# Optimization experiments

Measured on AMD Instinct MI355X. Metric: run time of the kernel, lower is better.

The kernel has to match this reference:

```python
import jax, jax.numpy as jnp
import numpy as np

NLAYERS, NHID, NOUT, BSZ, STEPS = 4, 1024, 512, 64, 128


def setup_inputs() -> dict:
    key = jax.random.key(0)
    k0, k1, k2, k3, k4 = jax.random.split(key, 5)
    stdv = 1.0 / np.sqrt(NHID).astype(np.float32)
    hx = jax.random.normal(k0, (NLAYERS, BSZ, NHID), jnp.float32)
    cx = jax.random.normal(k1, (NLAYERS, BSZ, NHID), jnp.float32)
    W = jax.random.uniform(k2, (NLAYERS - 1, 4 * NHID, NHID), jnp.float32, -stdv, stdv)
    U = jax.random.uniform(k3, (NLAYERS, 4 * NHID, NHID), jnp.float32, -stdv, stdv)
    L = jax.random.uniform(k4, (NOUT, NHID), jnp.float32, -stdv, stdv)
    return {"hx": hx, "cx": cx, "W": W, "U": U, "L": L, "steps": STEPS}


def _lstm_cell(igates, hgates, cx):
    # PyTorch fused LSTM gate order: input, forget, cell, output
    g = igates + hgates
    i, f, c, o = jnp.split(g, 4, axis=-1)
    i = jax.nn.sigmoid(i)
    f = jax.nn.sigmoid(f)
    c = jnp.tanh(c)
    o = jax.nn.sigmoid(o)
    cy = f * cx + i * c
    hy = o * jnp.tanh(cy)
    return hy, cy


def reference(hx, cx, W, U, L, steps):
    nlayers, bsz, nhid = hx.shape
    out0 = hx[-1] @ L.T  # initial projection of top-layer hidden -> [bsz, nout]

    def step(carry, _):
        h, c = carry
        # hidden-to-gate GEMM for all layers at once: [L,B,4H]
        hgates = jnp.einsum('lbh,lgh->lbg', h, U)
        hy_list, cy_list = [], []
        prev = jnp.zeros((bsz, 4 * nhid), h.dtype)  # layer-0 input gates are zeros
        for i in range(nlayers):
            igates = prev if i == 0 else hy_list[-1] @ W[i - 1].T
            hy, cy = _lstm_cell(igates, hgates[i], c[i])
            hy_list.append(hy)
            cy_list.append(cy)
        hn = jnp.stack(hy_list, 0)
        cn = jnp.stack(cy_list, 0)
        out = hy_list[-1] @ L.T  # [bsz, nout]
        return (hn, cn), out

    _, outs = jax.lax.scan(step, (hx, cx), None, length=steps - 1)
    return jnp.concatenate([out0[None], outs], axis=0)  # [steps, bsz, nout]
```

## Files before the change

kernel.cpp:

```cpp
#include <hip/hip_runtime.h>


#define H      1024
#define B      64
#define NL     4
#define BH     (B * H)
#define NOUTD  512
#define NSCAN  127
#define NWAVES 130
#define RSTR   36
#define KL     512

typedef __attribute__((ext_vector_type(8))) short short8;
typedef __attribute__((ext_vector_type(4))) float f32x4;

__device__ __forceinline__ unsigned short f2bf(float x) {
  union { float f; unsigned int u; } v; v.f = x;
  unsigned int r = v.u + 0x7FFFu + ((v.u >> 16) & 1u);
  return (unsigned short)(r >> 16);
}
__device__ __forceinline__ short8 pack8(float4 a, float4 b) {
  short8 r;
  r[0] = (short)f2bf(a.x); r[1] = (short)f2bf(a.y);
  r[2] = (short)f2bf(a.z); r[3] = (short)f2bf(a.w);
  r[4] = (short)f2bf(b.x); r[5] = (short)f2bf(b.y);
  r[6] = (short)f2bf(b.z); r[7] = (short)f2bf(b.w);
  return r;
}
__device__ __forceinline__ float sigmoidf_(float x) {
  return 1.0f / (1.0f + __expf(-x));
}
__device__ __forceinline__ float tanhf_(float x) {
  float ax = fabsf(x);
  float t = __expf(-2.0f * ax);
  float r = 1.0f - 2.0f * t / (1.0f + t);
  return copysignf(r, x);
}

__device__ __forceinline__ void ldg16(short8* d, const unsigned short* p) {
  asm volatile("global_load_dwordx4 %0, %1, off" : "=v"(*d) : "v"(p));
}
#define VMWAIT2 do { asm volatile("s_waitcnt vmcnt(2)" ::: "memory"); \
                     __builtin_amdgcn_sched_barrier(0); } while (0)
#define VMWAIT0 do { asm volatile("s_waitcnt vmcnt(0)" ::: "memory"); \
                     __builtin_amdgcn_sched_barrier(0); } while (0)

__device__ __forceinline__ void st_h4(unsigned short* p, unsigned v) {
  __hip_atomic_store((unsigned*)p, v, __ATOMIC_RELAXED, __HIP_MEMORY_SCOPE_AGENT);
}

__global__ __launch_bounds__(512, 2)
__attribute__((amdgpu_waves_per_eu(2, 2)))
void lstm_persist(
    const float* __restrict__ hx, const float* __restrict__ cx,
    const float* __restrict__ Wm, const float* __restrict__ Um,
    unsigned short* __restrict__ hmon, unsigned* __restrict__ flags) {
  __shared__ __align__(16) unsigned short WuL[64 * KL];
  __shared__ __align__(16) float red[4][64 * RSTR];
  __shared__ float cS[B * 16];

  const int tid = threadIdx.x;
  const int q = tid >> 6;
  const int lane = tid & 63;
  const int l15 = lane & 15;
  const int lhi = lane >> 4;
  const int bid = blockIdx.x;
  const int lyr = bid >> 6;
  const int jt = bid & 63;

#define HSL(l, p) (hmon + ((size_t)(l) * 128 + (size_t)((p) - (l))) * BH)
#define TOFF(b, col) (((size_t)((col) >> 5)) * 2048 + (size_t)(b) * 32 + ((col) & 31))
#define FROW(w) (flags + (size_t)(w) * 512)

  {
    const int u = tid * 2;
    const int b = u >> 4, jj = u & 15;
    const int C = jt * 16 + jj;
    const size_t gi = (size_t)lyr * BH + (size_t)b * H + C;
    const unsigned hv = (unsigned)f2bf(hx[gi]) | ((unsigned)f2bf(hx[gi + 1]) << 16);
    st_h4(HSL(lyr, lyr) + TOFF(b, C), hv);
    cS[b * 16 + jj] = cx[gi];
    cS[b * 16 + jj + 1] = cx[gi + 1];
  }

  {
    const int lr = tid >> 3;
    const int kb0 = (tid & 7) * 64;
    const int gr = (lr >> 4) * 1024 + jt * 16 + (lr & 15);
    const float* src = Um + ((size_t)lyr * 4096 + gr) * 1024 + kb0;
#pragma unroll
    for (int jc = 0; jc < 8; ++jc) {
      float4 f0 = *(const float4*)(src + jc * 8);
      float4 f1 = *(const float4*)(src + jc * 8 + 4);
      int byteoff = ((lr * KL + kb0 + jc * 8) * 2) ^ ((lr & 7) << 4);
      *(short8*)((char*)WuL + byteoff) = pack8(f0, f1);
    }
  }

  short8 wreg[6][4];
  if (lyr == 0) {
#pragma unroll
    for (int c = 0; c < 2; ++c) {
      const int kk = KL + 64 * q + 32 * c + 8 * lhi;
#pragma unroll
      for (int n = 0; n < 4; ++n) {
        const int gr = n * 1024 + jt * 16 + l15;
        const float* src = Um + (size_t)gr * 1024 + kk;
        wreg[c][n] = pack8(*(const float4*)src, *(const float4*)(src + 4));
      }
    }
  } else {
#pragma unroll
    for (int c = 0; c < 6; ++c) {
      const int kk = KL + 192 * q + 32 * c + 8 * lhi;
#pragma unroll
      for (int n = 0; n < 4; ++n) {
        const int gr = n * 1024 + jt * 16 + l15;
        const float* src = (kk < 1024)
            ? (Um + ((size_t)lyr * 4096 + gr) * 1024 + kk)
            : (Wm + ((size_t)(lyr - 1) * 4096 + gr) * 1024 + (kk - 1024));
        wreg[c][n] = pack8(*(const float4*)src, *(const float4*)(src + 4));
      }
    }
  }

  asm volatile("s_waitcnt vmcnt(0)" ::: "memory");
  __syncthreads();
  if (tid == 0) {
    __hip_atomic_store(FROW(0) + 0 * 256 + lyr * 64 + jt, 1u,
                       __ATOMIC_RELAXED, __HIP_MEMORY_SCOPE_AGENT);
    __hip_atomic_store(FROW(0) + 1 * 256 + lyr * 64 + jt, 1u,
                       __ATOMIC_RELAXED, __HIP_MEMORY_SCOPE_AGENT);
  }

  for (int w = 0; w < NWAVES; ++w) {
    const int s = w - lyr;
    const bool active = (s >= 0 && s < NSCAN);

#pragma unroll
    for (int half = 0; half < 2; ++half) {
      if (active) {
        {
          const unsigned* row = FROW(w) + half * 256;
          const unsigned* myf = nullptr;
          if (lyr > 0) {
            if (lane < 16) {
              int ll, blk;
              if (lane < 4) { ll = lyr; blk = 4 * q + lane; }
              else {
                const int r = 32 + 12 * q + (lane - 4);
                ll = (r >= 64) ? (lyr - 1) : lyr;
                blk = r & 63;
              }
              myf = row + ll * 64 + blk;
            }
          } else {
            if (lane < 8) {
              const int blk = (lane < 4) ? (4 * q + lane) : (32 + 4 * q + (lane - 4));
              myf = row + blk;
            }
          }
          if (myf)
            while (!__hip_atomic_load(myf, __ATOMIC_RELAXED, __HIP_MEMORY_SCOPE_AGENT))
              __builtin_amdgcn_s_sleep(1);
        }

        const unsigned short* aU = HSL(lyr, w) + (size_t)half * 1024
                                   + (size_t)l15 * 32 + lhi * 8;
        const unsigned short* aW = ((lyr > 0) ? HSL(lyr - 1, w) : HSL(lyr, w))
                                   + (size_t)half * 1024 + (size_t)l15 * 32 + lhi * 8;

        f32x4 acc[2][4];
#pragma unroll
        for (int m = 0; m < 2; ++m)
#pragma unroll
          for (int n = 0; n < 4; ++n) acc[m][n] = (f32x4){0.f, 0.f, 0.f, 0.f};

        short8 A2[2][2];

#define KSEL1(c)  ((c) < 2 ? (64 * q + 32 * (c)) : (KL + 192 * q + 32 * ((c) - 2)))
#define KSEL0(c)  ((c) < 2 ? (64 * q + 32 * (c)) : (KL + 64 * q + 32 * ((c) - 2)))
#define ISSUE(buf, k) { \
    const unsigned short* _p = ((k) < 1024) ? (aU + (size_t)((k) >> 5) * 2048) \
                                            : (aW + (size_t)(((k) - 1024) >> 5) * 2048); \
    ldg16(&A2[buf][0], _p); \
    ldg16(&A2[buf][1], _p + 512); }

        if (lyr > 0) {
          ISSUE(0, KSEL1(0));
          ISSUE(1, KSEL1(1));
#pragma unroll
          for (int c = 0; c < 8; ++c) {
            if (c < 7) VMWAIT2; else VMWAIT0;
            if (c < 2) {
              const int kk = 64 * q + 32 * c;
#pragma unroll
              for (int n = 0; n < 4; ++n) {
                const int byteoff = (((n * 16 + l15) * KL + kk + 8 * lhi) * 2) ^ ((l15 & 7) << 4);
                short8 bb = *(const short8*)((const char*)WuL + byteoff);
#pragma unroll
                for (int m = 0; m < 2; ++m)
                  acc[m][n] = __builtin_amdgcn_mfma_f32_16x16x32_bf16(A2[c & 1][m], bb, acc[m][n], 0, 0, 0);
              }
            } else {
#pragma unroll
              for (int n = 0; n < 4; ++n)
#pragma unroll
                for (int m = 0; m < 2; ++m)
                  acc[m][n] = __builtin_amdgcn_mfma_f32_16x16x32_bf16(A2[c & 1][m], wreg[c - 2][n], acc[m][n], 0, 0, 0);
            }
            if (c + 2 < 8) ISSUE(c & 1, KSEL1(c + 2));
          }
        } else {
          ISSUE(0, KSEL0(0));
          ISSUE(1, KSEL0(1));
#pragma unroll
          for (int c = 0; c < 4; ++c) {
            if (c < 3) VMWAIT2; else VMWAIT0;
            if (c < 2) {
              const int kk = 64 * q + 32 * c;
#pragma unroll
              for (int n = 0; n < 4; ++n) {
                const int byteoff = (((n * 16 + l15) * KL + kk + 8 * lhi) * 2) ^ ((l15 & 7) << 4);
                short8 bb = *(const short8*)((const char*)WuL + byteoff);
#pragma unroll
                for (int m = 0; m < 2; ++m)
                  acc[m][n] = __builtin_amdgcn_mfma_f32_16x16x32_bf16(A2[c & 1][m], bb, acc[m][n], 0, 0, 0);
              }
            } else {
#pragma unroll
              for (int n = 0; n < 4; ++n)
#pragma unroll
                for (int m = 0; m < 2; ++m)
                  acc[m][n] = __builtin_amdgcn_mfma_f32_16x16x32_bf16(A2[c & 1][m], wreg[c - 2][n], acc[m][n], 0, 0, 0);
            }
            if (c + 2 < 4) ISSUE(c & 1, KSEL0(c + 2));
          }
        }
#undef ISSUE
#undef KSEL1
#undef KSEL0

        {
          float* tile = red[q & 3];
          if (q < 4) {
#pragma unroll
            for (int m = 0; m < 2; ++m)
#pragma unroll
              for (int n = 0; n < 4; ++n)
                *(f32x4*)&tile[(n * 16 + l15) * RSTR + m * 16 + lhi * 4] = acc[m][n];
          }
          __syncthreads();
          if (q >= 4) {
#pragma unroll
            for (int m = 0; m < 2; ++m)
#pragma unroll
              for (int n = 0; n < 4; ++n) {
                float* p = &tile[(n * 16 + l15) * RSTR + m * 16 + lhi * 4];
                f32x4 v = *(f32x4*)p; v += acc[m][n]; *(f32x4*)p = v;
              }
          }
          __syncthreads();
        }

        if (tid < 256) {
          const int u = tid * 2;
          const int bl = u >> 4, jj = u & 15;
          const int b = bl + half * 32;
          const int C = jt * 16 + jj;
          unsigned short hyv[2];
#pragma unroll
          for (int e = 0; e < 2; ++e) {
            const int j2 = jj + e;
            float ig = 0.f, fg = 0.f, gg = 0.f, og = 0.f;
#pragma unroll
            for (int t = 0; t < 4; ++t) {
              ig += red[t][(0 * 16 + j2) * RSTR + bl];
              fg += red[t][(1 * 16 + j2) * RSTR + bl];
              gg += red[t][(2 * 16 + j2) * RSTR + bl];
              og += red[t][(3 * 16 + j2) * RSTR + bl];
            }
            const float i_ = sigmoidf_(ig);
            const float f_ = sigmoidf_(fg);
            const float g_ = tanhf_(gg);
            const float o_ = sigmoidf_(og);
            const float cv = f_ * cS[b * 16 + j2] + i_ * g_;
            cS[b * 16 + j2] = cv;
            hyv[e] = f2bf(o_ * tanhf_(cv));
          }
          st_h4(HSL(lyr, w + 1) + TOFF(b, C),
                (unsigned)hyv[0] | ((unsigned)hyv[1] << 16));
          asm volatile("s_waitcnt vmcnt(0)" ::: "memory");
        }
        __syncthreads();
        if (tid == 0)
          __hip_atomic_store(FROW(w + 1) + half * 256 + lyr * 64 + jt, 1u,
                             __ATOMIC_RELAXED, __HIP_MEMORY_SCOPE_AGENT);
      } else {
        if (tid == 0)
          __hip_atomic_store(FROW(w + 1) + half * 256 + lyr * 64 + jt, 1u,
                             __ATOMIC_RELAXED, __HIP_MEMORY_SCOPE_AGENT);
      }
    }
  }
#undef HSL
#undef TOFF
#undef FROW
}

__global__ __launch_bounds__(256) void proj_kernel(
    const unsigned short* __restrict__ hist, const float* __restrict__ Lm,
    float* __restrict__ out) {
  __shared__ __align__(16) unsigned short As[64 * 136];
  const int tid = threadIdx.x;
  const int q = tid >> 6;
  const int lane = tid & 63;
  const int l15 = lane & 15;
  const int lhi = lane >> 4;
  const int mt = blockIdx.x >> 3;
  const int nt = blockIdx.x & 7;

  f32x4 acc[4];
#pragma unroll
  for (int m = 0; m < 4; ++m) acc[m] = (f32x4){0.f, 0.f, 0.f, 0.f};

  for (int kb = 0; kb < 8; ++kb) {
    __syncthreads();
#pragma unroll
    for (int i = 0; i < 4; ++i) {
      int g = tid + 256 * i;
      int row = g >> 4, cu = g & 15;
      const int C = kb * 128 + cu * 8;
      *(short8*)(&As[row * 136 + cu * 8]) =
          *(const short8*)(&hist[(size_t)mt * 65536 + (size_t)(C >> 5) * 2048
                                 + (size_t)row * 32 + (C & 31)]);
    }
    __syncthreads();
#pragma unroll
    for (int kk = 0; kk < 4; ++kk) {
      const int ko = kk * 32 + 8 * lhi;
      const float* src = Lm + ((size_t)nt * 64 + q * 16 + l15) * H + kb * 128 + ko;
      short8 bb = pack8(*(const float4*)src, *(const float4*)(src + 4));
#pragma unroll
      for (int m = 0; m < 4; ++m) {
        short8 a = *(const short8*)(&As[(m * 16 + l15) * 136 + ko]);
        acc[m] = __builtin_amdgcn_mfma_f32_16x16x32_bf16(a, bb, acc[m], 0, 0, 0);
      }
    }
  }
  const int col = nt * 64 + q * 16 + l15;
#pragma unroll
  for (int m = 0; m < 4; ++m)
#pragma unroll
    for (int j = 0; j < 4; ++j) {
      const int row = mt * 64 + m * 16 + lhi * 4 + j;
      out[(size_t)row * NOUTD + col] = acc[m][j];
    }
}

extern "C" void kernel_launch(void* const* d_in, const int* in_sizes, int n_in,
                              void* d_out, int out_size, void* d_ws, size_t ws_size,
                              hipStream_t stream) {
  const float* hx = (const float*)d_in[0];
  const float* cx = (const float*)d_in[1];
  const float* Wm = (const float*)d_in[2];
  const float* Um = (const float*)d_in[3];
  const float* Lm = (const float*)d_in[4];
  float* out = (float*)d_out;

  char* ws = (char*)d_ws;
  unsigned* flags = (unsigned*)ws;
  unsigned short* hmon = (unsigned short*)(ws + (1 << 19));

  hipMemsetAsync(flags, 0, 1 << 19, stream);

  void* args[] = {(void*)&hx, (void*)&cx, (void*)&Wm, (void*)&Um,
                  (void*)&hmon, (void*)&flags};
  hipLaunchCooperativeKernel((const void*)lstm_persist, dim3(256), dim3(512),
                             args, 0, stream);
  const unsigned short* hist = hmon + (size_t)3 * 128 * BH;
  proj_kernel<<<dim3(1024), dim3(256), 0, stream>>>(hist, Lm, out);
}
```

Before: 1.043 ms.

## Prefetch next half-step's hidden-state tiles during current MFMA tail

Moves the dependency-flag wait and the first two A-operand global loads for the next half-step so they run during the last MFMA chunks of the current half-step. Those loads then overlap the reduction and LSTM epilogue instead of sitting serially at the start of each half-step. A `pref` flag lets the following iteration skip re-issuing loads that are already in flight. The cost is a spin-wait on flags inside the compute loop and register pressure from keeping the A buffers live across the epilogue, which could stall or lower occupancy.

```diff
diff --git a/kernel.cpp b/kernel.cpp
--- a/kernel.cpp
+++ b/kernel.cpp
@@ -133,113 +133,111 @@
                        __ATOMIC_RELAXED, __HIP_MEMORY_SCOPE_AGENT);
   }
 
+  short8 A2[2][2];
+
+#define WAITDEPS(rowbase) { \
+    const unsigned* _row = (rowbase); \
+    const unsigned* _myf = nullptr; \
+    if (lyr > 0) { \
+      if (lane < 16) { \
+        int _ll, _blk; \
+        if (lane < 4) { _ll = lyr; _blk = 4 * q + lane; } \
+        else { \
+          const int _r = 32 + 12 * q + (lane - 4); \
+          _ll = (_r >= 64) ? (lyr - 1) : lyr; \
+          _blk = _r & 63; \
+        } \
+        _myf = _row + _ll * 64 + _blk; \
+      } \
+    } else { \
+      if (lane < 8) { \
+        const int _blk = (lane < 4) ? (4 * q + lane) : (32 + 4 * q + (lane - 4)); \
+        _myf = _row + _blk; \
+      } \
+    } \
+    if (_myf) \
+      while (!__hip_atomic_load(_myf, __ATOMIC_RELAXED, __HIP_MEMORY_SCOPE_AGENT)) \
+        __builtin_amdgcn_s_sleep(1); }
+
+#define KSEL1(c)  ((c) < 2 ? (64 * q + 32 * (c)) : (KL + 192 * q + 32 * ((c) - 2)))
+#define KSEL0(c)  ((c) < 2 ? (64 * q + 32 * (c)) : (KL + 64 * q + 32 * ((c) - 2)))
+#define ISSUE(buf, ww, hh, k) { \
+    const unsigned short* _b = ((k) < 1024) \
+      ? (HSL(lyr, (ww)) + (size_t)(hh) * 1024 + (size_t)l15 * 32 + lhi * 8 \
+         + (size_t)((k) >> 5) * 2048) \
+      : (HSL(lyr - 1, (ww)) + (size_t)(hh) * 1024 + (size_t)l15 * 32 + lhi * 8 \
+         + (size_t)(((k) - 1024) >> 5) * 2048); \
+    ldg16(&A2[buf][0], _b); \
+    ldg16(&A2[buf][1], _b + 512); }
+#define CONSUME(c) { \
+    if ((c) < 2) { \
+      const int kk = 64 * q + 32 * (c); \
+      _Pragma("unroll") \
+      for (int n = 0; n < 4; ++n) { \
+        const int byteoff = (((n * 16 + l15) * KL + kk + 8 * lhi) * 2) ^ ((l15 & 7) << 4); \
+        short8 bb = *(const short8*)((const char*)WuL + byteoff); \
+        _Pragma("unroll") \
+        for (int m = 0; m < 2; ++m) \
+          acc[m][n] = __builtin_amdgcn_mfma_f32_16x16x32_bf16(A2[(c) & 1][m], bb, acc[m][n], 0, 0, 0); \
+      } \
+    } else { \
+      _Pragma("unroll") \
+      for (int n = 0; n < 4; ++n) \
+        _Pragma("unroll") \
+        for (int m = 0; m < 2; ++m) \
+          acc[m][n] = __builtin_amdgcn_mfma_f32_16x16x32_bf16(A2[(c) & 1][m], wreg[(c) - 2][n], acc[m][n], 0, 0, 0); \
+    } }
+
+  bool pref = false;
+
   for (int w = 0; w < NWAVES; ++w) {
     const int s = w - lyr;
     const bool active = (s >= 0 && s < NSCAN);
 
 #pragma unroll
     for (int half = 0; half < 2; ++half) {
+      const int nw = (half == 0) ? w : (w + 1);
+      const int nh = (half == 0) ? 1 : 0;
+      const bool nextActive = (half == 0) ? active
+                              : ((w + 1 - lyr) >= 0 && (w + 1 - lyr) < NSCAN);
       if (active) {
-        {
-          const unsigned* row = FROW(w) + half * 256;
-          const unsigned* myf = nullptr;
-          if (lyr > 0) {
-            if (lane < 16) {
-              int ll, blk;
-              if (lane < 4) { ll = lyr; blk = 4 * q + lane; }
-              else {
-                const int r = 32 + 12 * q + (lane - 4);
-                ll = (r >= 64) ? (lyr - 1) : lyr;
-                blk = r & 63;
-              }
-              myf = row + ll * 64 + blk;
+        if (!pref) {
+          WAITDEPS(FROW(w) + half * 256);
+          if (lyr > 0) { ISSUE(0, w, half, KSEL1(0)); ISSUE(1, w, half, KSEL1(1)); }
+          else         { ISSUE(0, w, half, KSEL0(0)); ISSUE(1, w, half, KSEL0(1)); }
+        }
+
+        f32x4 acc[2][4];
+#pragma unroll
+        for (int m = 0; m < 2; ++m)
+#pragma unroll
+          for (int n = 0; n < 4; ++n) acc[m][n] = (f32x4){0.f, 0.f, 0.f, 0.f};
+
+        if (lyr > 0) {
+#pragma unroll
+          for (int c = 0; c < 8; ++c) {
+            if (c == 7 && !nextActive) { VMWAIT0; } else { VMWAIT2; }
+            CONSUME(c);
+            if (c + 2 < 8) { ISSUE(c & 1, w, half, KSEL1(c + 2)); }
+            else if (c == 6) {
+              if (nextActive) { WAITDEPS(FROW(nw) + nh * 256); ISSUE(0, nw, nh, KSEL1(0)); }
+            } else {
+              if (nextActive) ISSUE(1, nw, nh, KSEL1(1));
             }
-          } else {
-            if (lane < 8) {
-              const int blk = (lane < 4) ? (4 * q + lane) : (32 + 4 * q + (lane - 4));
-              myf = row + blk;
+          }
+        } else {
+#pragma unroll
+          for (int c = 0; c < 4; ++c) {
+            if (c == 3 && !nextActive) { VMWAIT0; } else { VMWAIT2; }
+            CONSUME(c);
+            if (c + 2 < 4) { ISSUE(c & 1, w, half, KSEL0(c + 2)); }
+            else if (c == 2) {
+              if (nextActive) { WAITDEPS(FROW(nw) + nh * 256); ISSUE(0, nw, nh, KSEL0(0)); }
+            } else {
+              if (nextActive) ISSUE(1, nw, nh, KSEL0(1));
             }
           }
-          if (myf)
-            while (!__hip_atomic_load(myf, __ATOMIC_RELAXED, __HIP_MEMORY_SCOPE_AGENT))
-              __builtin_amdgcn_s_sleep(1);
         }
-
-        const unsigned short* aU = HSL(lyr, w) + (size_t)half * 1024
-                                   + (size_t)l15 * 32 + lhi * 8;
-        const unsigned short* aW = ((lyr > 0) ? HSL(lyr - 1, w) : HSL(lyr, w))
-                                   + (size_t)half * 1024 + (size_t)l15 * 32 + lhi * 8;
-
-        f32x4 acc[2][4];
-#pragma unroll
-        for (int m = 0; m < 2; ++m)
-#pragma unroll
-          for (int n = 0; n < 4; ++n) acc[m][n] = (f32x4){0.f, 0.f, 0.f, 0.f};
-
-        short8 A2[2][2];
-
-#define KSEL1(c)  ((c) < 2 ? (64 * q + 32 * (c)) : (KL + 192 * q + 32 * ((c) - 2)))
-#define KSEL0(c)  ((c) < 2 ? (64 * q + 32 * (c)) : (KL + 64 * q + 32 * ((c) - 2)))
-#define ISSUE(buf, k) { \
-    const unsigned short* _p = ((k) < 1024) ? (aU + (size_t)((k) >> 5) * 2048) \
-                                            : (aW + (size_t)(((k) - 1024) >> 5) * 2048); \
-    ldg16(&A2[buf][0], _p); \
-    ldg16(&A2[buf][1], _p + 512); }
-
-        if (lyr > 0) {
-          ISSUE(0, KSEL1(0));
-          ISSUE(1, KSEL1(1));
-#pragma unroll
-          for (int c = 0; c < 8; ++c) {
-            if (c < 7) VMWAIT2; else VMWAIT0;
-            if (c < 2) {
-              const int kk = 64 * q + 32 * c;
-#pragma unroll
-              for (int n = 0; n < 4; ++n) {
-                const int byteoff = (((n * 16 + l15) * KL + kk + 8 * lhi) * 2) ^ ((l15 & 7) << 4);
-                short8 bb = *(const short8*)((const char*)WuL + byteoff);
-#pragma unroll
-                for (int m = 0; m < 2; ++m)
-                  acc[m][n] = __builtin_amdgcn_mfma_f32_16x16x32_bf16(A2[c & 1][m], bb, acc[m][n], 0, 0, 0);
-              }
-            } else {
-#pragma unroll
-              for (int n = 0; n < 4; ++n)
-#pragma unroll
-                for (int m = 0; m < 2; ++m)
-                  acc[m][n] = __builtin_amdgcn_mfma_f32_16x16x32_bf16(A2[c & 1][m], wreg[c - 2][n], acc[m][n], 0, 0, 0);
-            }
-            if (c + 2 < 8) ISSUE(c & 1, KSEL1(c + 2));
-          }
-        } else {
-          ISSUE(0, KSEL0(0));
-          ISSUE(1, KSEL0(1));
-#pragma unroll
-          for (int c = 0; c < 4; ++c) {
-            if (c < 3) VMWAIT2; else VMWAIT0;
-            if (c < 2) {
-              const int kk = 64 * q + 32 * c;
-#pragma unroll
-              for (int n = 0; n < 4; ++n) {
-                const int byteoff = (((n * 16 + l15) * KL + kk + 8 * lhi) * 2) ^ ((l15 & 7) << 4);
-                short8 bb = *(const short8*)((const char*)WuL + byteoff);
-#pragma unroll
-                for (int m = 0; m < 2; ++m)
-                  acc[m][n] = __builtin_amdgcn_mfma_f32_16x16x32_bf16(A2[c & 1][m], bb, acc[m][n], 0, 0, 0);
-              }
-            } else {
-#pragma unroll
-              for (int n = 0; n < 4; ++n)
-#pragma unroll
-                for (int m = 0; m < 2; ++m)
-                  acc[m][n] = __builtin_amdgcn_mfma_f32_16x16x32_bf16(A2[c & 1][m], wreg[c - 2][n], acc[m][n], 0, 0, 0);
-            }
-            if (c + 2 < 4) ISSUE(c & 1, KSEL0(c + 2));
-          }
-        }
-#undef ISSUE
-#undef KSEL1
-#undef KSEL0
 
         {
           float* tile = red[q & 3];
@@ -296,16 +294,23 @@
         if (tid == 0)
           __hip_atomic_store(FROW(w + 1) + half * 256 + lyr * 64 + jt, 1u,
                              __ATOMIC_RELAXED, __HIP_MEMORY_SCOPE_AGENT);
+        pref = nextActive;
       } else {
         if (tid == 0)
           __hip_atomic_store(FROW(w + 1) + half * 256 + lyr * 64 + jt, 1u,
                              __ATOMIC_RELAXED, __HIP_MEMORY_SCOPE_AGENT);
+        pref = false;
       }
     }
   }
 #undef HSL
 #undef TOFF
 #undef FROW
+#undef WAITDEPS
+#undef KSEL1
+#undef KSEL0
+#undef ISSUE
+#undef CONSUME
 }
 
 __global__ __launch_bounds__(256) void proj_kernel(
```

Result: faster. 927.4 us (-11.1%).
